# Optimization experiments

Hardware: AMD Instinct MI355X
Metric: run time of the kernel (lower is better)

The kernel has to match this reference:

```python
import jax, jax.numpy as jnp
import numpy as np

D_MODEL = 128
N_HEADS = 8
D_K = D_MODEL // N_HEADS
N_NODES = 50000
N_EDGES = 800000


def setup_inputs() -> dict:
    key = jax.random.key(0)
    ks = jax.random.split(key, 8)
    X = jax.random.normal(ks[0], (N_NODES, D_MODEL), dtype=jnp.float32)
    nbr_src = jax.random.randint(ks[1], (N_EDGES,), 0, N_NODES, dtype=jnp.int32)
    nbr_dst = jax.random.randint(ks[2], (N_EDGES,), 0, N_NODES, dtype=jnp.int32)
    s = 1.0 / np.sqrt(D_MODEL)
    W_qkv = jax.random.normal(ks[3], (3 * D_MODEL, D_MODEL), dtype=jnp.float32) * s
    w_bias = jax.random.normal(ks[4], (N_HEADS, D_MODEL), dtype=jnp.float32) * s
    W_gate = jax.random.normal(ks[5], (D_MODEL, D_MODEL), dtype=jnp.float32) * s
    b_gate = jax.random.normal(ks[6], (D_MODEL,), dtype=jnp.float32) * s
    W_o = jax.random.normal(ks[7], (D_MODEL, D_MODEL), dtype=jnp.float32) * s
    return {"X": X, "W_qkv": W_qkv, "w_bias": w_bias, "W_gate": W_gate,
            "b_gate": b_gate, "W_o": W_o, "nbr_src": nbr_src,
            "nbr_dst": nbr_dst, "num_cells": N_NODES}


def segment_softmax(scores, seg, num_segments):
    # scores: [E, H], seg: [E] -> softmax over edges sharing the same seg id
    mx = jax.ops.segment_max(scores, seg, num_segments=num_segments)  # [N, H]
    mx = jnp.where(jnp.isfinite(mx), mx, -1e9)
    exp_s = jnp.exp(scores - mx[seg])
    sm = jax.ops.segment_sum(exp_s, seg, num_segments=num_segments)  # [N, H]
    return exp_s / (sm[seg] + 1e-12)


def reference(X, W_qkv, w_bias, W_gate, b_gate, W_o, nbr_src, nbr_dst, num_cells):
    H, dk = N_HEADS, D_K
    scale = 1.0 / np.sqrt(dk)
    qkv = (X @ W_qkv.T).reshape(-1, 3, H, dk)      # [N, 3, H, dk]
    Q, K, V = qkv[:, 0], qkv[:, 1], qkv[:, 2]
    gate = jax.nn.sigmoid(X @ W_gate.T + b_gate).reshape(-1, H, dk)
    bias = X @ w_bias.T                             # [N, H]
    scores = jnp.einsum('ehd,ehd->eh', Q[nbr_src], K[nbr_dst]) * scale + bias[nbr_src]
    attn = segment_softmax(scores, nbr_src, num_cells)          # [E, H]
    out = jax.ops.segment_sum(attn[:, :, None] * V[nbr_dst], nbr_src,
                              num_segments=num_cells)           # [N, H, dk]
    return (gate * out).reshape(-1, D_MODEL) @ W_o.T
```

## Files before the change

kernel.cpp:

```cpp
#include <hip/hip_runtime.h>
#include <hip/hip_fp16.h>

#define DM 128
#define NHEADS 8
#define MAXDEG 64
#define SROW 136

typedef _Float16 half8 __attribute__((ext_vector_type(8)));
typedef _Float16 half2v __attribute__((ext_vector_type(2)));
typedef float floatx4 __attribute__((ext_vector_type(4)));

union H8 { half8 v; half2v h2[4]; };

__global__ __launch_bounds__(256) void proj_csr(
    const float* __restrict__ X, const float* __restrict__ Wqkv,
    const float* __restrict__ Wgate, const float* __restrict__ wbias,
    const float* __restrict__ b_gate,
    const int* __restrict__ nsrc, const int* __restrict__ ndst,
    int* __restrict__ cnt, int* __restrict__ csr_dst,
    _Float16* __restrict__ Q, _Float16* __restrict__ KV,
    _Float16* __restrict__ gate, float* __restrict__ bias,
    int M, int E, int P) {
  __shared__ _Float16 As[128 * SROW];
  __shared__ _Float16 Bs[64 * SROW];
  int tid = threadIdx.x;
  int bid = blockIdx.x;

  if (bid >= P) {
    int ebase = (bid - P) * 8192;
    for (int g = 0; g < 4; g++) {
      int s[8], d[8];
#pragma unroll
      for (int j = 0; j < 8; j++) {
        int e = ebase + (g * 8 + j) * 256 + tid;
        s[j] = (e < E) ? nsrc[e] : -1;
        d[j] = (e < E) ? ndst[e] : 0;
      }
#pragma unroll
      for (int j = 0; j < 8; j++) {
        if (s[j] >= 0) {
          int p = atomicAdd(&cnt[s[j]], 1);
          if (p < MAXDEG) csr_dst[(size_t)s[j] * MAXDEG + p] = d[j];
        }
      }
    }
    return;
  }

  int m0 = bid * 128;

#pragma unroll
  for (int i = 0; i < 4; i++) {
    int u = tid + i * 256;
    int r = u >> 3;
    int cc = (u & 7) * 16;
    int gr = m0 + r;
    float4 f0, f1, f2, f3;
    if (gr < M) {
      const float4* src = (const float4*)(X + (size_t)gr * 128 + cc);
      f0 = src[0]; f1 = src[1]; f2 = src[2]; f3 = src[3];
    } else {
      f0 = f1 = f2 = f3 = make_float4(0.f, 0.f, 0.f, 0.f);
    }
    half8 h0 = {(_Float16)f0.x, (_Float16)f0.y, (_Float16)f0.z, (_Float16)f0.w,
                (_Float16)f1.x, (_Float16)f1.y, (_Float16)f1.z, (_Float16)f1.w};
    half8 h1 = {(_Float16)f2.x, (_Float16)f2.y, (_Float16)f2.z, (_Float16)f2.w,
                (_Float16)f3.x, (_Float16)f3.y, (_Float16)f3.z, (_Float16)f3.w};
    *(half8*)(As + r * SROW + cc) = h0;
    *(half8*)(As + r * SROW + cc + 8) = h1;
  }

  int wid = tid >> 6, lane = tid & 63;
  int quad = lane >> 4, l16 = lane & 15;
  int mw = wid * 32;

  float bg0[4], bg1[4];
#pragma unroll
  for (int ni = 0; ni < 4; ni++) {
    bg0[ni] = b_gate[ni * 16 + l16];
    bg1[ni] = b_gate[64 + ni * 16 + l16];
  }

  for (int c = 0; c < 9; c++) {
    __syncthreads();
#pragma unroll
    for (int i = 0; i < 4; i++) {
      int u = tid + i * 256;
      int r = u >> 4;
      int cc = (u & 15) * 8;
      int grow = c * 64 + r;
      const float* src = nullptr;
      if (grow < 384)      src = Wqkv + (size_t)grow * 128 + cc;
      else if (grow < 512) src = Wgate + (size_t)(grow - 384) * 128 + cc;
      else if (grow < 520) src = wbias + (size_t)(grow - 512) * 128 + cc;
      half8 h = {};
      if (src) {
        float4 f0 = ((const float4*)src)[0];
        float4 f1 = ((const float4*)src)[1];
        h = half8{(_Float16)f0.x, (_Float16)f0.y, (_Float16)f0.z, (_Float16)f0.w,
                  (_Float16)f1.x, (_Float16)f1.y, (_Float16)f1.z, (_Float16)f1.w};
      }
      *(half8*)(Bs + r * SROW + cc) = h;
    }
    __syncthreads();

    floatx4 acc[2][4] = {};
#pragma unroll
    for (int kc = 0; kc < 4; kc++) {
      int ko = kc * 32 + quad * 8;
      half8 a0 = *(const half8*)(As + (mw + l16) * SROW + ko);
      half8 a1 = *(const half8*)(As + (mw + 16 + l16) * SROW + ko);
      half8 b[4];
#pragma unroll
      for (int ni = 0; ni < 4; ni++)
        b[ni] = *(const half8*)(Bs + (ni * 16 + l16) * SROW + ko);
#pragma unroll
      for (int ni = 0; ni < 4; ni++) {
        acc[0][ni] = __builtin_amdgcn_mfma_f32_16x16x32_f16(a0, b[ni], acc[0][ni], 0, 0, 0);
        acc[1][ni] = __builtin_amdgcn_mfma_f32_16x16x32_f16(a1, b[ni], acc[1][ni], 0, 0, 0);
      }
    }

    if (c == 8) {
      if (l16 < 8) {
#pragma unroll
        for (int mi = 0; mi < 2; mi++)
#pragma unroll
          for (int r = 0; r < 4; r++) {
            int row = m0 + mw + mi * 16 + quad * 4 + r;
            if (row < M) bias[(size_t)row * 8 + l16] = acc[mi][0][r];
          }
      }
    } else {
      int reg = c >> 1;
#pragma unroll
      for (int mi = 0; mi < 2; mi++) {
#pragma unroll
        for (int ni = 0; ni < 4; ni++) {
          int colL = (c & 1) * 64 + ni * 16 + l16;
          float bgv = (c & 1) ? bg1[ni] : bg0[ni];
#pragma unroll
          for (int r = 0; r < 4; r++) {
            int row = m0 + mw + mi * 16 + quad * 4 + r;
            if (row >= M) continue;
            float v = acc[mi][ni][r];
            if (reg == 0)      Q[(size_t)row * 128 + colL] = (_Float16)v;
            else if (reg == 1) KV[(size_t)row * 256 + colL] = (_Float16)v;
            else if (reg == 2) KV[(size_t)row * 256 + 128 + colL] = (_Float16)v;
            else gate[(size_t)row * 128 + colL] =
                   (_Float16)(1.0f / (1.0f + __expf(-(v + bgv))));
          }
        }
      }
    }
  }
}

__global__ __launch_bounds__(256) void final_gemm_mfma(
    const _Float16* __restrict__ A, const float* __restrict__ Wo,
    float* __restrict__ C, int M) {
  __shared__ _Float16 As[128 * SROW];
  __shared__ _Float16 Bs[64 * SROW];
  int tid = threadIdx.x;
  int m0 = blockIdx.x * 128, n0 = blockIdx.y * 64;
#pragma unroll
  for (int i = 0; i < 8; i++) {
    int u = tid + i * 256;
    int r = u >> 4;
    int cc = (u & 15) * 8;
    int gr = m0 + r;
    int4 val = make_int4(0, 0, 0, 0);
    if (gr < M) val = *(const int4*)(A + (size_t)gr * 128 + cc);
    *(int4*)(As + r * SROW + cc) = val;
  }
#pragma unroll
  for (int i = 0; i < 4; i++) {
    int u = tid + i * 256;
    int r = u >> 4;
    int cc = (u & 15) * 8;
    const float* src = Wo + (size_t)(n0 + r) * 128 + cc;
    float4 f0 = ((const float4*)src)[0];
    float4 f1 = ((const float4*)src)[1];
    half8 h = {(_Float16)f0.x, (_Float16)f0.y, (_Float16)f0.z, (_Float16)f0.w,
               (_Float16)f1.x, (_Float16)f1.y, (_Float16)f1.z, (_Float16)f1.w};
    *(half8*)(Bs + r * SROW + cc) = h;
  }
  __syncthreads();

  int wid = tid >> 6, lane = tid & 63;
  int quad = lane >> 4, l16 = lane & 15;
  int mw = (wid >> 1) * 64;
  int nw = (wid & 1) * 32;

  floatx4 acc[4][2] = {};
#pragma unroll
  for (int kc = 0; kc < 4; kc++) {
    int ko = kc * 32 + quad * 8;
    half8 a[4], b[2];
#pragma unroll
    for (int mi = 0; mi < 4; mi++)
      a[mi] = *(const half8*)(As + (mw + mi * 16 + l16) * SROW + ko);
#pragma unroll
    for (int ni = 0; ni < 2; ni++)
      b[ni] = *(const half8*)(Bs + (nw + ni * 16 + l16) * SROW + ko);
#pragma unroll
    for (int mi = 0; mi < 4; mi++)
#pragma unroll
      for (int ni = 0; ni < 2; ni++)
        acc[mi][ni] = __builtin_amdgcn_mfma_f32_16x16x32_f16(a[mi], b[ni], acc[mi][ni], 0, 0, 0);
  }
#pragma unroll
  for (int mi = 0; mi < 4; mi++) {
#pragma unroll
    for (int ni = 0; ni < 2; ni++) {
      int col = n0 + nw + ni * 16 + l16;
#pragma unroll
      for (int r = 0; r < 4; r++) {
        int row = m0 + mw + mi * 16 + quad * 4 + r;
        if (row >= M) continue;
        C[(size_t)row * 128 + col] = acc[mi][ni][r];
      }
    }
  }
}

__global__ __launch_bounds__(256) void attn_fused(
    const int* __restrict__ cnt, const int* __restrict__ csr_dst,
    const _Float16* __restrict__ Q, const _Float16* __restrict__ KV,
    const float* __restrict__ bias, const _Float16* __restrict__ gate,
    _Float16* __restrict__ gated, int N) {
  int wave = threadIdx.x >> 6, lane = threadIdx.x & 63;
  int n = blockIdx.x * 4 + wave;
  if (n >= N) return;
  int deg = __builtin_nontemporal_load(cnt + n);
  if (deg > MAXDEG) deg = MAXDEG;
  int qtr = lane >> 4, l16 = lane & 15;
  int ch0 = l16 * 8;

  int dstv = __builtin_nontemporal_load(csr_dst + (size_t)n * MAXDEG + lane);

  H8 qu; qu.v = __builtin_nontemporal_load((const half8*)(Q + (size_t)n * DM + ch0));
  float bias_h = __builtin_nontemporal_load(bias + (size_t)n * NHEADS + (l16 >> 1));

  float acc[8] = {};
  float den = 0.f;
  int iters = (deg + 3) >> 2;

  H8 kb[4], vb[4];
  bool bb[4];
#pragma unroll
  for (int j = 0; j < 4; j++) {
    bb[j] = false;
    kb[j].v = half8{}; vb[j].v = half8{};
    if (j < iters) {
      int e = j * 4 + qtr;
      bb[j] = e < deg;
      int d = __shfl(dstv, e);
      d = bb[j] ? d : 0;
      const _Float16* kvp = KV + (size_t)d * 256 + ch0;
      kb[j].v = *(const half8*)kvp;
      vb[j].v = *(const half8*)(kvp + 128);
    }
  }

  for (int base = 0; base < iters; base += 4) {
#pragma unroll
    for (int j = 0; j < 4; j++) {
      float p = 0.f;
#pragma unroll
      for (int t = 0; t < 4; t++)
        p = __builtin_amdgcn_fdot2(qu.h2[t], kb[j].h2[t], p, false);
      p += __shfl_xor(p, 1);
      float w = __expf(p * 0.25f + bias_h);
      if (!bb[j]) w = 0.f;
      den += w;
#pragma unroll
      for (int t = 0; t < 8; t++) acc[t] = fmaf(w, (float)vb[j].v[t], acc[t]);
      int idx = base + 4 + j;
      bb[j] = false;
      if (idx < iters) {
        int e = idx * 4 + qtr;
        bb[j] = e < deg;
        int d = __shfl(dstv, e);
        d = bb[j] ? d : 0;
        const _Float16* kvp = KV + (size_t)d * 256 + ch0;
        kb[j].v = *(const half8*)kvp;
        vb[j].v = *(const half8*)(kvp + 128);
      }
    }
  }

#pragma unroll
  for (int j = 0; j < 8; j++) acc[j] += __shfl_xor(acc[j], 16);
#pragma unroll
  for (int j = 0; j < 8; j++) acc[j] += __shfl_xor(acc[j], 32);
  den += __shfl_xor(den, 16);
  den += __shfl_xor(den, 32);

  if (qtr == 0) {
    float inv = 1.0f / (den + 1e-12f);
    half8 gv = __builtin_nontemporal_load((const half8*)(gate + (size_t)n * DM + ch0));
    half8 o;
#pragma unroll
    for (int j = 0; j < 8; j++) o[j] = (_Float16)(acc[j] * inv * (float)gv[j]);
    *(half8*)(gated + (size_t)n * DM + ch0) = o;
  }
}

extern "C" void kernel_launch(void* const* d_in, const int* in_sizes, int n_in,
                              void* d_out, int out_size, void* d_ws, size_t ws_size,
                              hipStream_t stream) {
  const float* X     = (const float*)d_in[0];
  const float* Wqkv  = (const float*)d_in[1];
  const float* wbias = (const float*)d_in[2];
  const float* Wgate = (const float*)d_in[3];
  const float* bgate = (const float*)d_in[4];
  const float* Wo    = (const float*)d_in[5];
  const int*   nsrc  = (const int*)d_in[6];
  const int*   ndst  = (const int*)d_in[7];
  int N = in_sizes[0] / 128;
  int E = in_sizes[6];
  float* out = (float*)d_out;

  char* p = (char*)d_ws;
  _Float16* Q16     = (_Float16*)p; p += (size_t)N * 128 * sizeof(_Float16);
  _Float16* KV16    = (_Float16*)p; p += (size_t)N * 256 * sizeof(_Float16);
  _Float16* gate16  = (_Float16*)p; p += (size_t)N * 128 * sizeof(_Float16);
  _Float16* gated16 = (_Float16*)p; p += (size_t)N * 128 * sizeof(_Float16);
  float* bias       = (float*)p;    p += (size_t)N * 8 * sizeof(float);
  int* cnt          = (int*)p;      p += (size_t)N * sizeof(int);
  int* csr_dst      = (int*)p;      p += (size_t)N * MAXDEG * sizeof(int);

  hipMemsetAsync(cnt, 0, (size_t)N * sizeof(int), stream);

  int P = (N + 127) / 128;
  int C = (E + 8191) / 8192;
  proj_csr<<<P + C, 256, 0, stream>>>(X, Wqkv, Wgate, wbias, bgate, nsrc, ndst,
                                      cnt, csr_dst, Q16, KV16, gate16, bias, N, E, P);

  attn_fused<<<(N + 3) / 4, 256, 0, stream>>>(cnt, csr_dst, Q16, KV16, bias,
                                              gate16, gated16, N);

  dim3 fg((N + 127) / 128, 2);
  final_gemm_mfma<<<fg, 256, 0, stream>>>(gated16, Wo, out, N);
}
```

Before: 217.2 us.

## Double-buffer weight tiles in projection kernel and schedule CSR blocks first

The projection kernel now double-buffers the weight tile in shared memory. It prefetches the next 64-row chunk of weights into registers while the MFMA work on the current chunk runs, and drops one of the two barriers per chunk. The CSR-building blocks are moved to the start of the grid so their atomic-heavy work is dispatched before the GEMM blocks. Shared memory use per block goes up and register pressure rises from the prefetch buffers, which may lower occupancy.

```diff
diff --git a/kernel.cpp b/kernel.cpp
--- a/kernel.cpp
+++ b/kernel.cpp
@@ -5,12 +5,18 @@
 #define NHEADS 8
 #define MAXDEG 64
 #define SROW 136
+#define BSZ (64 * SROW)
 
 typedef _Float16 half8 __attribute__((ext_vector_type(8)));
 typedef _Float16 half2v __attribute__((ext_vector_type(2)));
 typedef float floatx4 __attribute__((ext_vector_type(4)));
 
 union H8 { half8 v; half2v h2[4]; };
+
+__device__ __forceinline__ half8 cvt_h8(float4 f0, float4 f1) {
+  return half8{(_Float16)f0.x, (_Float16)f0.y, (_Float16)f0.z, (_Float16)f0.w,
+               (_Float16)f1.x, (_Float16)f1.y, (_Float16)f1.z, (_Float16)f1.w};
+}
 
 __global__ __launch_bounds__(256) void proj_csr(
     const float* __restrict__ X, const float* __restrict__ Wqkv,
@@ -20,14 +26,14 @@
     int* __restrict__ cnt, int* __restrict__ csr_dst,
     _Float16* __restrict__ Q, _Float16* __restrict__ KV,
     _Float16* __restrict__ gate, float* __restrict__ bias,
-    int M, int E, int P) {
+    int M, int E, int C) {
   __shared__ _Float16 As[128 * SROW];
-  __shared__ _Float16 Bs[64 * SROW];
+  __shared__ _Float16 Bs[2 * BSZ];
   int tid = threadIdx.x;
   int bid = blockIdx.x;
 
-  if (bid >= P) {
-    int ebase = (bid - P) * 8192;
+  if (bid < C) {
+    int ebase = bid * 8192;
     for (int g = 0; g < 4; g++) {
       int s[8], d[8];
 #pragma unroll
@@ -47,7 +53,8 @@
     return;
   }
 
-  int m0 = bid * 128;
+  int pbid = bid - C;
+  int m0 = pbid * 128;
 
 #pragma unroll
   for (int i = 0; i < 4; i++) {
@@ -62,12 +69,19 @@
     } else {
       f0 = f1 = f2 = f3 = make_float4(0.f, 0.f, 0.f, 0.f);
     }
-    half8 h0 = {(_Float16)f0.x, (_Float16)f0.y, (_Float16)f0.z, (_Float16)f0.w,
-                (_Float16)f1.x, (_Float16)f1.y, (_Float16)f1.z, (_Float16)f1.w};
-    half8 h1 = {(_Float16)f2.x, (_Float16)f2.y, (_Float16)f2.z, (_Float16)f2.w,
-                (_Float16)f3.x, (_Float16)f3.y, (_Float16)f3.z, (_Float16)f3.w};
-    *(half8*)(As + r * SROW + cc) = h0;
-    *(half8*)(As + r * SROW + cc + 8) = h1;
+    *(half8*)(As + r * SROW + cc) = cvt_h8(f0, f1);
+    *(half8*)(As + r * SROW + cc + 8) = cvt_h8(f2, f3);
+  }
+
+#pragma unroll
+  for (int i = 0; i < 4; i++) {
+    int u = tid + i * 256;
+    int r = u >> 4;
+    int cc = (u & 15) * 8;
+    const float* src = Wqkv + (size_t)r * 128 + cc;
+    float4 f0 = ((const float4*)src)[0];
+    float4 f1 = ((const float4*)src)[1];
+    *(half8*)(Bs + r * SROW + cc) = cvt_h8(f0, f1);
   }
 
   int wid = tid >> 6, lane = tid & 63;
@@ -81,28 +95,29 @@
     bg1[ni] = b_gate[64 + ni * 16 + l16];
   }
 
+  __syncthreads();
+
   for (int c = 0; c < 9; c++) {
-    __syncthreads();
-#pragma unroll
-    for (int i = 0; i < 4; i++) {
-      int u = tid + i * 256;
-      int r = u >> 4;
-      int cc = (u & 15) * 8;
-      int grow = c * 64 + r;
-      const float* src = nullptr;
-      if (grow < 384)      src = Wqkv + (size_t)grow * 128 + cc;
-      else if (grow < 512) src = Wgate + (size_t)(grow - 384) * 128 + cc;
-      else if (grow < 520) src = wbias + (size_t)(grow - 512) * 128 + cc;
-      half8 h = {};
-      if (src) {
-        float4 f0 = ((const float4*)src)[0];
-        float4 f1 = ((const float4*)src)[1];
-        h = half8{(_Float16)f0.x, (_Float16)f0.y, (_Float16)f0.z, (_Float16)f0.w,
-                  (_Float16)f1.x, (_Float16)f1.y, (_Float16)f1.z, (_Float16)f1.w};
-      }
-      *(half8*)(Bs + r * SROW + cc) = h;
-    }
-    __syncthreads();
+    const _Float16* Bcur = Bs + (c & 1) * BSZ;
+    _Float16* Bnxt = Bs + ((c + 1) & 1) * BSZ;
+
+    float4 pf0[4], pf1[4];
+    if (c < 8) {
+#pragma unroll
+      for (int i = 0; i < 4; i++) {
+        int u = tid + i * 256;
+        int r = u >> 4;
+        int cc = (u & 15) * 8;
+        int grow = (c + 1) * 64 + r;
+        const float* src = nullptr;
+        if (grow < 384)      src = Wqkv + (size_t)grow * 128 + cc;
+        else if (grow < 512) src = Wgate + (size_t)(grow - 384) * 128 + cc;
+        else if (grow < 520) src = wbias + (size_t)(grow - 512) * 128 + cc;
+        if (src) { pf0[i] = ((const float4*)src)[0]; pf1[i] = ((const float4*)src)[1]; }
+        else { pf0[i] = make_float4(0.f, 0.f, 0.f, 0.f); pf1[i] = pf0[i]; }
+      }
+      __builtin_amdgcn_sched_barrier(0);
+    }
 
     floatx4 acc[2][4] = {};
 #pragma unroll
@@ -113,7 +128,7 @@
       half8 b[4];
 #pragma unroll
       for (int ni = 0; ni < 4; ni++)
-        b[ni] = *(const half8*)(Bs + (ni * 16 + l16) * SROW + ko);
+        b[ni] = *(const half8*)(Bcur + (ni * 16 + l16) * SROW + ko);
 #pragma unroll
       for (int ni = 0; ni < 4; ni++) {
         acc[0][ni] = __builtin_amdgcn_mfma_f32_16x16x32_f16(a0, b[ni], acc[0][ni], 0, 0, 0);
@@ -153,6 +168,17 @@
         }
       }
     }
+
+    if (c < 8) {
+#pragma unroll
+      for (int i = 0; i < 4; i++) {
+        int u = tid + i * 256;
+        int r = u >> 4;
+        int cc = (u & 15) * 8;
+        *(half8*)(Bnxt + r * SROW + cc) = cvt_h8(pf0[i], pf1[i]);
+      }
+      __syncthreads();
+    }
   }
 }
 
@@ -181,9 +207,7 @@
     const float* src = Wo + (size_t)(n0 + r) * 128 + cc;
     float4 f0 = ((const float4*)src)[0];
     float4 f1 = ((const float4*)src)[1];
-    half8 h = {(_Float16)f0.x, (_Float16)f0.y, (_Float16)f0.z, (_Float16)f0.w,
-               (_Float16)f1.x, (_Float16)f1.y, (_Float16)f1.z, (_Float16)f1.w};
-    *(half8*)(Bs + r * SROW + cc) = h;
+    *(half8*)(Bs + r * SROW + cc) = cvt_h8(f0, f1);
   }
   __syncthreads();
 
@@ -335,8 +359,8 @@
 
   int P = (N + 127) / 128;
   int C = (E + 8191) / 8192;
-  proj_csr<<<P + C, 256, 0, stream>>>(X, Wqkv, Wgate, wbias, bgate, nsrc, ndst,
-                                      cnt, csr_dst, Q16, KV16, gate16, bias, N, E, P);
+  proj_csr<<<C + P, 256, 0, stream>>>(X, Wqkv, Wgate, wbias, bgate, nsrc, ndst,
+                                      cnt, csr_dst, Q16, KV16, gate16, bias, N, E, C);
 
   attn_fused<<<(N + 3) / 4, 256, 0, stream>>>(cnt, csr_dst, Q16, KV16, bias,
                                               gate16, gated16, N);
```

Result: slower. 227.3 us (+4.7%).

## Rewrite output GEMM as persistent kernel with LDS-resident weight, A from registers

Applied to the files above, without the earlier changes.

The final projection kernel now loads the full converted W_o into LDS once per block and runs a persistent grid of 512 blocks. Each wave loops over 16-row tiles, reading A fragments straight from global memory into registers and computing all 128 output columns. This removes the per-tile A staging through LDS and the repeated W_o fp32-to-fp16 conversion across a 2D grid. In exchange each tile issues direct uncoalesced-ish 16-byte global loads and has fewer waves in flight to hide them. A small conversion helper also replaces the duplicated inline conversions.

```diff
diff --git a/kernel.cpp b/kernel.cpp
--- a/kernel.cpp
+++ b/kernel.cpp
@@ -5,12 +5,18 @@
 #define NHEADS 8
 #define MAXDEG 64
 #define SROW 136
+#define FSTRIDE 132
 
 typedef _Float16 half8 __attribute__((ext_vector_type(8)));
 typedef _Float16 half2v __attribute__((ext_vector_type(2)));
 typedef float floatx4 __attribute__((ext_vector_type(4)));
 
 union H8 { half8 v; half2v h2[4]; };
+
+__device__ __forceinline__ half8 cvt_h8(float4 f0, float4 f1) {
+  return half8{(_Float16)f0.x, (_Float16)f0.y, (_Float16)f0.z, (_Float16)f0.w,
+               (_Float16)f1.x, (_Float16)f1.y, (_Float16)f1.z, (_Float16)f1.w};
+}
 
 __global__ __launch_bounds__(256) void proj_csr(
     const float* __restrict__ X, const float* __restrict__ Wqkv,
@@ -62,12 +68,8 @@
     } else {
       f0 = f1 = f2 = f3 = make_float4(0.f, 0.f, 0.f, 0.f);
     }
-    half8 h0 = {(_Float16)f0.x, (_Float16)f0.y, (_Float16)f0.z, (_Float16)f0.w,
-                (_Float16)f1.x, (_Float16)f1.y, (_Float16)f1.z, (_Float16)f1.w};
-    half8 h1 = {(_Float16)f2.x, (_Float16)f2.y, (_Float16)f2.z, (_Float16)f2.w,
-                (_Float16)f3.x, (_Float16)f3.y, (_Float16)f3.z, (_Float16)f3.w};
-    *(half8*)(As + r * SROW + cc) = h0;
-    *(half8*)(As + r * SROW + cc + 8) = h1;
+    *(half8*)(As + r * SROW + cc) = cvt_h8(f0, f1);
+    *(half8*)(As + r * SROW + cc + 8) = cvt_h8(f2, f3);
   }
 
   int wid = tid >> 6, lane = tid & 63;
@@ -97,8 +99,7 @@
       if (src) {
         float4 f0 = ((const float4*)src)[0];
         float4 f1 = ((const float4*)src)[1];
-        h = half8{(_Float16)f0.x, (_Float16)f0.y, (_Float16)f0.z, (_Float16)f0.w,
-                  (_Float16)f1.x, (_Float16)f1.y, (_Float16)f1.z, (_Float16)f1.w};
+        h = cvt_h8(f0, f1);
       }
       *(half8*)(Bs + r * SROW + cc) = h;
     }
@@ -156,69 +157,54 @@
   }
 }
 
-__global__ __launch_bounds__(256) void final_gemm_mfma(
+__global__ __launch_bounds__(256) void final_gemm_reg(
     const _Float16* __restrict__ A, const float* __restrict__ Wo,
     float* __restrict__ C, int M) {
-  __shared__ _Float16 As[128 * SROW];
-  __shared__ _Float16 Bs[64 * SROW];
+  __shared__ _Float16 Ws[128 * FSTRIDE];
   int tid = threadIdx.x;
-  int m0 = blockIdx.x * 128, n0 = blockIdx.y * 64;
 #pragma unroll
   for (int i = 0; i < 8; i++) {
     int u = tid + i * 256;
     int r = u >> 4;
     int cc = (u & 15) * 8;
-    int gr = m0 + r;
-    int4 val = make_int4(0, 0, 0, 0);
-    if (gr < M) val = *(const int4*)(A + (size_t)gr * 128 + cc);
-    *(int4*)(As + r * SROW + cc) = val;
-  }
-#pragma unroll
-  for (int i = 0; i < 4; i++) {
-    int u = tid + i * 256;
-    int r = u >> 4;
-    int cc = (u & 15) * 8;
-    const float* src = Wo + (size_t)(n0 + r) * 128 + cc;
+    const float* src = Wo + (size_t)r * 128 + cc;
     float4 f0 = ((const float4*)src)[0];
     float4 f1 = ((const float4*)src)[1];
-    half8 h = {(_Float16)f0.x, (_Float16)f0.y, (_Float16)f0.z, (_Float16)f0.w,
-               (_Float16)f1.x, (_Float16)f1.y, (_Float16)f1.z, (_Float16)f1.w};
-    *(half8*)(Bs + r * SROW + cc) = h;
+    *(half8*)(Ws + r * FSTRIDE + cc) = cvt_h8(f0, f1);
   }
   __syncthreads();
 
   int wid = tid >> 6, lane = tid & 63;
   int quad = lane >> 4, l16 = lane & 15;
-  int mw = (wid >> 1) * 64;
-  int nw = (wid & 1) * 32;
-
-  floatx4 acc[4][2] = {};
-#pragma unroll
-  for (int kc = 0; kc < 4; kc++) {
-    int ko = kc * 32 + quad * 8;
-    half8 a[4], b[2];
-#pragma unroll
-    for (int mi = 0; mi < 4; mi++)
-      a[mi] = *(const half8*)(As + (mw + mi * 16 + l16) * SROW + ko);
-#pragma unroll
-    for (int ni = 0; ni < 2; ni++)
-      b[ni] = *(const half8*)(Bs + (nw + ni * 16 + l16) * SROW + ko);
-#pragma unroll
-    for (int mi = 0; mi < 4; mi++)
-#pragma unroll
-      for (int ni = 0; ni < 2; ni++)
-        acc[mi][ni] = __builtin_amdgcn_mfma_f32_16x16x32_f16(a[mi], b[ni], acc[mi][ni], 0, 0, 0);
-  }
-#pragma unroll
-  for (int mi = 0; mi < 4; mi++) {
-#pragma unroll
-    for (int ni = 0; ni < 2; ni++) {
-      int col = n0 + nw + ni * 16 + l16;
+  int tiles = (M + 15) >> 4;
+  int gw = blockIdx.x * 4 + wid;
+  int nw = gridDim.x * 4;
+
+  for (int t = gw; t < tiles; t += nw) {
+    int r0 = t * 16;
+    int arow = r0 + l16;
+    half8 af[4];
+#pragma unroll
+    for (int kc = 0; kc < 4; kc++)
+      af[kc] = (arow < M) ? *(const half8*)(A + (size_t)arow * 128 + kc * 32 + quad * 8)
+                          : half8{};
+    floatx4 acc[8] = {};
+#pragma unroll
+    for (int kc = 0; kc < 4; kc++) {
+      int ko = kc * 32 + quad * 8;
+#pragma unroll
+      for (int ni = 0; ni < 8; ni++) {
+        half8 bf = *(const half8*)(Ws + (ni * 16 + l16) * FSTRIDE + ko);
+        acc[ni] = __builtin_amdgcn_mfma_f32_16x16x32_f16(af[kc], bf, acc[ni], 0, 0, 0);
+      }
+    }
+#pragma unroll
+    for (int ni = 0; ni < 8; ni++) {
+      int col = ni * 16 + l16;
 #pragma unroll
       for (int r = 0; r < 4; r++) {
-        int row = m0 + mw + mi * 16 + quad * 4 + r;
-        if (row >= M) continue;
-        C[(size_t)row * 128 + col] = acc[mi][ni][r];
+        int row = r0 + quad * 4 + r;
+        if (row < M) C[(size_t)row * 128 + col] = acc[ni][r];
       }
     }
   }
@@ -341,6 +327,5 @@
   attn_fused<<<(N + 3) / 4, 256, 0, stream>>>(cnt, csr_dst, Q16, KV16, bias,
                                               gate16, gated16, N);
 
-  dim3 fg((N + 127) / 128, 2);
-  final_gemm_mfma<<<fg, 256, 0, stream>>>(gated16, Wo, out, N);
-}
+  final_gemm_reg<<<512, 256, 0, stream>>>(gated16, Wo, out, N);
+}
```

Measured after the change: 217.2 us. Within noise of the previous version (-0.0%).
